# Optimization experiments

Measured on AMD Instinct MI355X. Metric: run time of the kernel, lower is better.

## Reference

```python
import jax, jax.numpy as jnp
import numpy as np


def setup_inputs() -> dict:
    key = jax.random.key(0)
    ks = jax.random.split(key, 5)
    B, T, C = 2, 2048, 1024
    x = jax.random.normal(ks[0], (B, T, C), dtype=jnp.float32)
    Wqkv = jax.random.normal(ks[1], (C, 3 * C), dtype=jnp.float32) * (C ** -0.5)
    bqkv = jax.random.normal(ks[2], (3 * C,), dtype=jnp.float32) * 0.02
    Wproj = jax.random.normal(ks[3], (C, C), dtype=jnp.float32) * (C ** -0.5)
    bproj = jax.random.normal(ks[4], (C,), dtype=jnp.float32) * 0.02
    return {"x": x, "Wqkv": Wqkv, "bqkv": bqkv, "Wproj": Wproj, "bproj": bproj}


def reference(x, Wqkv, bqkv, Wproj, bproj):
    B, T, C = x.shape
    n_head = 16
    hd = C // n_head
    x_proj = x @ Wqkv + bqkv  # [B, T, 3C]
    # NOTE: source reshapes (B, T, C) -> (B, n_head, T, hd) directly (no transpose);
    # we replicate that exactly for faithfulness.
    q = x_proj[:, :, :C].reshape(B, n_head, T, hd)
    k = x_proj[:, :, C:2 * C].reshape(B, n_head, T, hd)
    v = x_proj[:, :, 2 * C:].reshape(B, n_head, T, hd)
    att = jnp.einsum('bhtd,bhsd->bhts', q, k) * (1.0 / jnp.sqrt(jnp.float32(hd)))
    causal = jnp.tril(jnp.ones((T, T), dtype=bool))  # True where allowed
    att = jnp.where(causal, att, jnp.float32(-jnp.inf))
    att = jax.nn.softmax(att, axis=-1)
    y = att @ v  # [B, H, T, hd]
    y = jnp.transpose(y, (0, 2, 1, 3)).reshape(B, T, C)
    return y @ Wproj + bproj
```

## Files before the change

### kernel.cpp

```cpp
#include <hip/hip_runtime.h>
#include <hip/hip_bf16.h>
#include <stdint.h>

typedef __hip_bfloat16 bf16;
typedef __attribute__((ext_vector_type(8))) short bf16x8;
typedef __attribute__((ext_vector_type(4))) float f32x4;

__device__ __forceinline__ bf16x8 ldsv8(const bf16* p) { return *(const bf16x8*)p; }

__device__ __forceinline__ short bf_bits(float f) {
  union { bf16 h; short s; } u; u.h = __float2bfloat16(f); return u.s;
}

#define QSCALE 0.18033688011112042f

#define ASYNC16(ldsdst, gsrc)                                                  \
  __builtin_amdgcn_global_load_lds(                                            \
      (const __attribute__((address_space(1))) void*)(gsrc),                   \
      (__attribute__((address_space(3))) void*)(ldsdst), 16, 0, 0)

__device__ __forceinline__ bool is_bf16(const void* p) {
  const uint32_t* w = (const uint32_t*)p;
  int cnt = 0;
#pragma unroll 8
  for (int i = 0; i < 64; ++i) {
    uint32_t e = (w[i] >> 7) & 0xffu;
    cnt += (e >= 100u && e <= 150u) ? 1 : 0;
  }
  return cnt >= 40;
}

__device__ __forceinline__ float load_f32(const void* p, size_t idx, bool b16) {
  return b16 ? __bfloat162float(((const bf16*)p)[idx]) : ((const float*)p)[idx];
}

__device__ __forceinline__ void cvtT_body(const void* in, bf16* out, int R,
                                          int Ccols, int bx, int by,
                                          bf16 (*tile)[33]) {
  const bool b16 = is_bf16(in);
  int tx = threadIdx.x & 31, ty = threadIdx.x >> 5;
  int c0 = bx * 32, r0 = by * 32;
#pragma unroll
  for (int i = 0; i < 32; i += 8)
    tile[ty + i][tx] = __float2bfloat16(load_f32(in, (size_t)(r0 + ty + i) * Ccols + c0 + tx, b16));
  __syncthreads();
#pragma unroll
  for (int i = 0; i < 32; i += 8)
    out[(size_t)(c0 + ty + i) * R + r0 + tx] = tile[tx][ty + i];
}

__global__ __launch_bounds__(256) void prep_k(const float* __restrict__ x,
                                              bf16* __restrict__ xb,
                                              const void* __restrict__ Wqkv,
                                              bf16* __restrict__ WqkvT,
                                              const void* __restrict__ Wproj,
                                              bf16* __restrict__ WprojT) {
  __shared__ __align__(16) bf16 tile[32][33];
  const int id = blockIdx.x;
  if (id < 2048) {
    size_t i = (size_t)id * 256 + threadIdx.x;
    const float4 f0 = ((const float4*)x)[i * 2];
    const float4 f1 = ((const float4*)x)[i * 2 + 1];
    bf16x8 pk = {bf_bits(f0.x), bf_bits(f0.y), bf_bits(f0.z), bf_bits(f0.w),
                 bf_bits(f1.x), bf_bits(f1.y), bf_bits(f1.z), bf_bits(f1.w)};
    ((bf16x8*)xb)[i] = pk;
  } else if (id < 5120) {
    int id2 = id - 2048;
    cvtT_body(Wqkv, WqkvT, 1024, 3072, id2 % 96, id2 / 96, tile);
  } else {
    int id3 = id - 5120;
    cvtT_body(Wproj, WprojT, 1024, 1024, id3 % 32, id3 / 32, tile);
  }
}

__global__ __launch_bounds__(256) void cvtT_k(const void* __restrict__ in,
                                              bf16* __restrict__ out,
                                              int R, int Ccols) {
  __shared__ __align__(16) bf16 tile[32][33];
  cvtT_body(in, out, R, Ccols, blockIdx.x, blockIdx.y, tile);
}

__global__ __launch_bounds__(256) void cvt_k(const float* __restrict__ in,
                                             bf16* __restrict__ out) {
  size_t i = (size_t)blockIdx.x * 256 + threadIdx.x;
  const float4 f0 = ((const float4*)in)[i * 2];
  const float4 f1 = ((const float4*)in)[i * 2 + 1];
  bf16x8 pk = {bf_bits(f0.x), bf_bits(f0.y), bf_bits(f0.z), bf_bits(f0.w),
               bf_bits(f1.x), bf_bits(f1.y), bf_bits(f1.z), bf_bits(f1.w)};
  ((bf16x8*)out)[i] = pk;
}

template <int MODE, int BN>
__global__ __launch_bounds__(256) void gemm128(
    const void* __restrict__ Araw, const bf16* __restrict__ BT,
    const void* __restrict__ biasraw, void* __restrict__ outv) {
  constexpr int K = 1024;
  constexpr int NBF = BN / 32;
  __shared__ __align__(16) bf16 As[128 * 32];
  __shared__ __align__(16) bf16 Bs[BN * 32];
  const int tid = threadIdx.x;
  const int wave = tid >> 6, lane = tid & 63;
  const int quad = lane >> 4, l16 = lane & 15;
  const int nwg = gridDim.x * gridDim.y;
  const int lin = blockIdx.y * gridDim.x + blockIdx.x;
  const int swz = (lin & 7) * (nwg >> 3) + (lin >> 3);
  const int m0 = (swz / gridDim.y) * 128, n0 = (swz % gridDim.y) * BN;
  const int wm = (wave & 1) * 64, wn = (wave >> 1) * (BN / 2);
  const bool a16 = (MODE == 0) ? is_bf16(Araw) : true;
  const bool bias16 = is_bf16(biasraw);

  f32x4 acc[4][NBF] = {};

  for (int kt = 0; kt < K; kt += 32) {
    __syncthreads();
    if (MODE != 0 || a16) {
#pragma unroll
      for (int i = 0; i < 2; ++i) {
        int slot = i * 256 + tid;
        int row = slot >> 2, col = (slot & 3) << 3;
        ASYNC16(As + slot * 8, ((const bf16*)Araw) + (size_t)(m0 + row) * K + kt + col);
      }
#pragma unroll
      for (int i = 0; i < BN / 64; ++i) {
        int slot = i * 256 + tid;
        int row = slot >> 2, col = (slot & 3) << 3;
        ASYNC16(Bs + slot * 8, BT + (size_t)(n0 + row) * K + kt + col);
      }
    } else {
#pragma unroll
      for (int i = 0; i < 2; ++i) {
        int slot = i * 256 + tid;
        int row = slot >> 2, col = (slot & 3) << 3;
        const float* ap = ((const float*)Araw) + (size_t)(m0 + row) * K + kt + col;
        float4 f0 = *(const float4*)ap;
        float4 f1 = *(const float4*)(ap + 4);
        bf16x8 pk = {bf_bits(f0.x), bf_bits(f0.y), bf_bits(f0.z), bf_bits(f0.w),
                     bf_bits(f1.x), bf_bits(f1.y), bf_bits(f1.z), bf_bits(f1.w)};
        *(bf16x8*)(As + slot * 8) = pk;
        if (i * 256 < BN * 4)
          *(bf16x8*)(Bs + slot * 8) = *(const bf16x8*)(BT + (size_t)(n0 + row) * K + kt + col);
      }
    }
    __syncthreads();
    bf16x8 af[4], bfr[NBF];
#pragma unroll
    for (int i = 0; i < 4; ++i)
      af[i] = ldsv8(As + (wm + i * 16 + l16) * 32 + quad * 8);
#pragma unroll
    for (int j = 0; j < NBF; ++j)
      bfr[j] = ldsv8(Bs + (wn + j * 16 + l16) * 32 + quad * 8);
#pragma unroll
    for (int i = 0; i < 4; ++i)
#pragma unroll
      for (int j = 0; j < NBF; ++j)
        acc[i][j] = __builtin_amdgcn_mfma_f32_16x16x32_bf16(af[i], bfr[j], acc[i][j], 0, 0, 0);
  }

  float biasf[NBF];
#pragma unroll
  for (int j = 0; j < NBF; ++j)
    biasf[j] = load_f32(biasraw, n0 + wn + j * 16 + l16, bias16);

#pragma unroll
  for (int i = 0; i < 4; ++i)
#pragma unroll
    for (int j = 0; j < NBF; ++j) {
      int ng = n0 + wn + j * 16 + l16;
#pragma unroll
      for (int r = 0; r < 4; ++r) {
        int mg = m0 + wm + i * 16 + quad * 4 + r;
        float v = acc[i][j][r] + biasf[j];
        if (MODE == 1) {
          ((float*)outv)[(size_t)mg * 1024 + ng] = v;
        } else {
          ((bf16*)outv)[(size_t)mg * 3072 + ng] =
              __float2bfloat16(ng < 1024 ? v * QSCALE : v);
        }
      }
    }
}

__global__ __launch_bounds__(1024, 4) void attn_k(const bf16* __restrict__ xproj,
                                                  bf16* __restrict__ Yb) {
  constexpr int KSZ = 128 * 72;
  constexpr int VSZ = 64 * 136;
  __shared__ __align__(16) bf16 Ks[2 * KSZ];
  __shared__ __align__(16) bf16 VTs[2 * VSZ];
  __shared__ __align__(16) bf16 Ps[16 * 16 * 136];

  const int tid = threadIdx.x;
  const int wave = tid >> 6, lane = tid & 63;
  const int quad = lane >> 4, l16 = lane & 15;
  const int tl = wave >> 3;
  const int wrow = (wave & 7) * 16;
  const int pid = blockIdx.x;
  const int qtA = pid, qtB = 15 - pid;
  const int qt = tl ? qtB : qtA;
  const int bh = blockIdx.y, b = bh >> 4, h = bh & 15;
  const size_t rowbase = (size_t)(b * 2048 + h * 128) * 3072;
  const int q0 = qt * 128;

  const short onebits = (short)0x3F80;
  const bf16x8 vones = {onebits, onebits, onebits, onebits,
                        onebits, onebits, onebits, onebits};

  bf16x8 aq[2];
  {
    int sg = q0 + wrow + l16;
    const bf16* qp = xproj + rowbase + (size_t)(sg >> 4) * 3072 + ((sg & 15) << 6);
#pragma unroll
    for (int ks = 0; ks < 2; ++ks)
      aq[ks] = *(const bf16x8*)(qp + ks * 32 + quad * 8);
  }

  f32x4 o[4] = {};
  f32x4 lacc = {};

  bf16* Pw = Ps + wave * (16 * 136);

  const int sA = tid >> 3, blkA = tid & 7;

  bf16x8 kreg, vreg;
#define ISSUE_LOADS(stv)                                                        \
  {                                                                             \
    int sg0 = (stv)*128 + sA;                                                   \
    const bf16* b0 = xproj + rowbase + (size_t)(sg0 >> 4) * 3072 + ((sg0 & 15) << 6); \
    kreg = *(const bf16x8*)(b0 + 1024 + blkA * 8);                              \
    vreg = *(const bf16x8*)(b0 + 2048 + blkA * 8);                              \
  }
#define WRITE_TILE(buf)                                                         \
  {                                                                             \
    bf16* Kd = Ks + (buf)*KSZ;                                                  \
    bf16* Vd = VTs + (buf)*VSZ;                                                 \
    *(bf16x8*)(Kd + sA * 72 + blkA * 8) = kreg;                                 \
    const bf16* vv = (const bf16*)&vreg;                                        \
    const int ssw = sA ^ (blkA << 3);                                           \
    _Pragma("unroll")                                                           \
    for (int j = 0; j < 8; ++j) Vd[(blkA * 8 + j) * 136 + ssw] = vv[j];         \
  }

  ISSUE_LOADS(0);
  WRITE_TILE(0);
  ISSUE_LOADS(1);
  __syncthreads();

  int cur = 0;
  for (int st = 0; st <= qtB; ++st) {
    const bf16* Kc = Ks + cur * KSZ;
    const bf16* Vc = VTs + cur * VSZ;

    if (st <= qt) {
      const bool diag = (st == qt);

      f32x4 sc[8] = {};
      __builtin_amdgcn_s_setprio(1);
#pragma unroll
      for (int ks = 0; ks < 2; ++ks)
#pragma unroll
        for (int j = 0; j < 8; ++j) {
          bf16x8 bk = ldsv8(Kc + (j * 16 + l16) * 72 + (ks * 4 + quad) * 8);
          sc[j] = __builtin_amdgcn_mfma_f32_16x16x32_bf16(aq[ks], bk, sc[j], 0, 0, 0);
        }
      __builtin_amdgcn_s_setprio(0);

#pragma unroll
      for (int r = 0; r < 4; ++r) {
        const int rloc = wrow + quad * 4 + r;
        bf16* prow = Pw + (quad * 4 + r) * 136;
        const int psw = quad << 3;
#pragma unroll
        for (int j = 0; j < 8; ++j) {
          float v = sc[j][r];
          if (diag && (j * 16 + l16) > rloc) v = -1e30f;
          prow[(j * 16 + l16) ^ psw] = __float2bfloat16(__builtin_amdgcn_exp2f(v));
        }
      }

      __builtin_amdgcn_s_setprio(1);
#pragma unroll
      for (int ks = 0; ks < 4; ++ks) {
        bf16x8 ap = ldsv8(Pw + l16 * 136 + (((ks * 4 + quad) ^ (l16 >> 2)) << 3));
        lacc = __builtin_amdgcn_mfma_f32_16x16x32_bf16(ap, vones, lacc, 0, 0, 0);
#pragma unroll
        for (int j = 0; j < 4; ++j) {
          int d = j * 16 + l16;
          bf16x8 bv = ldsv8(Vc + d * 136 + (((ks * 4 + quad) ^ (2 * j + (l16 >> 3))) << 3));
          o[j] = __builtin_amdgcn_mfma_f32_16x16x32_bf16(ap, bv, o[j], 0, 0, 0);
        }
      }
      __builtin_amdgcn_s_setprio(0);
    }

    if (st < qtB) {
      WRITE_TILE(cur ^ 1);
      if (st + 2 <= qtB) ISSUE_LOADS(st + 2);
      __syncthreads();
      cur ^= 1;
    }
  }
#undef ISSUE_LOADS
#undef WRITE_TILE

  bf16* Yh = Yb + (size_t)b * 2097152 + h * 64;
#pragma unroll
  for (int r = 0; r < 4; ++r) {
    int tt = q0 + wrow + quad * 4 + r;
    float inv = 1.f / lacc[r];
#pragma unroll
    for (int j = 0; j < 4; ++j)
      Yh[(size_t)tt * 1024 + j * 16 + l16] = __float2bfloat16(o[j][r] * inv);
  }
}

extern "C" void kernel_launch(void* const* d_in, const int* in_sizes, int n_in,
                              void* d_out, int out_size, void* d_ws, size_t ws_size,
                              hipStream_t stream) {
  (void)out_size;
  const void* px     = d_in[0];
  const void* pWqkv  = (n_in > 1) ? d_in[1] : d_in[0];
  const void* pbqkv  = (n_in > 2) ? d_in[2] : d_in[0];
  const void* pWproj = (n_in > 3) ? d_in[3] : d_in[0];
  const void* pbproj = (n_in > 4) ? d_in[4] : d_in[0];
  for (int i = 0; i < n_in; ++i) {
    switch (in_sizes[i]) {
      case 4194304: px     = d_in[i]; break;
      case 3145728: pWqkv  = d_in[i]; break;
      case 3072:    pbqkv  = d_in[i]; break;
      case 1048576: pWproj = d_in[i]; break;
      case 1024:    pbproj = d_in[i]; break;
      default: break;
    }
  }

  char* ws = (char*)d_ws;
  bf16* xproj = (bf16*)(ws + 0);

  if (ws_size >= 41943040) {
    bf16* xb     = (bf16*)(ws + 25165824);
    bf16* WqkvT  = (bf16*)(ws + 33554432);
    bf16* WprojT = (bf16*)(ws + 39845888);
    bf16* Yb     = (bf16*)(ws + 27262976);

    prep_k<<<dim3(6144), 256, 0, stream>>>((const float*)px, xb, pWqkv, WqkvT,
                                           pWproj, WprojT);
    gemm128<0, 128><<<dim3(32, 24), 256, 0, stream>>>(xb, WqkvT, pbqkv, xproj);
    attn_k<<<dim3(8, 32), 1024, 0, stream>>>(xproj, Yb);
    gemm128<1, 64><<<dim3(32, 16), 256, 0, stream>>>(Yb, WprojT, pbproj, d_out);
  } else if (ws_size >= 39845888) {
    bf16* xb     = (bf16*)(ws + 25165824);
    bf16* WqkvT  = (bf16*)(ws + 33554432);
    bf16* WprojT = (bf16*)(ws + 25165824);
    bf16* Yb     = (bf16*)(ws + 27262976);

    cvt_k<<<dim3(2048), 256, 0, stream>>>((const float*)px, xb);
    cvtT_k<<<dim3(96, 32), 256, 0, stream>>>(pWqkv, WqkvT, 1024, 3072);
    gemm128<0, 128><<<dim3(32, 24), 256, 0, stream>>>(xb, WqkvT, pbqkv, xproj);
    cvtT_k<<<dim3(32, 32), 256, 0, stream>>>(pWproj, WprojT, 1024, 1024);
    attn_k<<<dim3(8, 32), 1024, 0, stream>>>(xproj, Yb);
    gemm128<1, 64><<<dim3(32, 16), 256, 0, stream>>>(Yb, WprojT, pbproj, d_out);
  } else {
    bf16* WqkvT  = (bf16*)(ws + 25165824);
    bf16* WprojT = (bf16*)(ws + 25165824);
    bf16* Yb     = (bf16*)(ws + 27262976);

    cvtT_k<<<dim3(96, 32), 256, 0, stream>>>(pWqkv, WqkvT, 1024, 3072);
    gemm128<0, 128><<<dim3(32, 24), 256, 0, stream>>>(px, WqkvT, pbqkv, xproj);
    cvtT_k<<<dim3(32, 32), 256, 0, stream>>>(pWproj, WprojT, 1024, 1024);
    attn_k<<<dim3(8, 32), 1024, 0, stream>>>(xproj, Yb);
    gemm128<1, 64><<<dim3(32, 16), 256, 0, stream>>>(Yb, WprojT, pbproj, d_out);
  }
}
```

Baseline: 186.8 us.

## Split long-tile key range across both wave groups after short tile finishes

Previously one half of the block processed the short query tile and then sat idle while the other half finished the long tile. Now the first group writes its short-tile result early, reloads Q for the long tile, and both groups then split each remaining key tile by 64-key halves. Partial outputs and row sums are combined through shared memory at the end. This is meant to remove the load imbalance between wave groups, at the cost of an extra reduction, extra syncs and narrower MFMA work per tile.

```diff
diff --git a/kernel.cpp b/kernel.cpp
--- a/kernel.cpp
+++ b/kernel.cpp
@@ -195,10 +195,8 @@
   const int wrow = (wave & 7) * 16;
   const int pid = blockIdx.x;
   const int qtA = pid, qtB = 15 - pid;
-  const int qt = tl ? qtB : qtA;
   const int bh = blockIdx.y, b = bh >> 4, h = bh & 15;
   const size_t rowbase = (size_t)(b * 2048 + h * 128) * 3072;
-  const int q0 = qt * 128;
 
   const short onebits = (short)0x3F80;
   const bf16x8 vones = {onebits, onebits, onebits, onebits,
@@ -206,7 +204,7 @@
 
   bf16x8 aq[2];
   {
-    int sg = q0 + wrow + l16;
+    int sg = (tl ? qtB : qtA) * 128 + wrow + l16;
     const bf16* qp = xproj + rowbase + (size_t)(sg >> 4) * 3072 + ((sg & 15) << 6);
 #pragma unroll
     for (int ks = 0; ks < 2; ++ks)
@@ -217,6 +215,7 @@
   f32x4 lacc = {};
 
   bf16* Pw = Ps + wave * (16 * 136);
+  bf16* Yh = Yb + (size_t)b * 2097152 + h * 64;
 
   const int sA = tid >> 3, blkA = tid & 7;
 
@@ -249,8 +248,8 @@
     const bf16* Kc = Ks + cur * KSZ;
     const bf16* Vc = VTs + cur * VSZ;
 
-    if (st <= qt) {
-      const bool diag = (st == qt);
+    if (st <= pid) {
+      const bool diag = (tl == 0) && (st == qtA);
 
       f32x4 sc[8] = {};
       __builtin_amdgcn_s_setprio(1);
@@ -279,6 +278,68 @@
       __builtin_amdgcn_s_setprio(1);
 #pragma unroll
       for (int ks = 0; ks < 4; ++ks) {
+        bf16x8 ap = ldsv8(Pw + l16 * 136 + (((ks * 4 + quad) ^ (l16 >> 2)) << 3));
+        lacc = __builtin_amdgcn_mfma_f32_16x16x32_bf16(ap, vones, lacc, 0, 0, 0);
+#pragma unroll
+        for (int j = 0; j < 4; ++j) {
+          int d = j * 16 + l16;
+          bf16x8 bv = ldsv8(Vc + d * 136 + (((ks * 4 + quad) ^ (2 * j + (l16 >> 3))) << 3));
+          o[j] = __builtin_amdgcn_mfma_f32_16x16x32_bf16(ap, bv, o[j], 0, 0, 0);
+        }
+      }
+      __builtin_amdgcn_s_setprio(0);
+
+      if (st == pid && tl == 0) {
+#pragma unroll
+        for (int r = 0; r < 4; ++r) {
+          int tt = qtA * 128 + wrow + quad * 4 + r;
+          float inv = 1.f / lacc[r];
+#pragma unroll
+          for (int j = 0; j < 4; ++j)
+            Yh[(size_t)tt * 1024 + j * 16 + l16] = __float2bfloat16(o[j][r] * inv);
+        }
+        int sg = qtB * 128 + wrow + l16;
+        const bf16* qp = xproj + rowbase + (size_t)(sg >> 4) * 3072 + ((sg & 15) << 6);
+#pragma unroll
+        for (int ks = 0; ks < 2; ++ks)
+          aq[ks] = *(const bf16x8*)(qp + ks * 32 + quad * 8);
+#pragma unroll
+        for (int j = 0; j < 4; ++j) o[j] = (f32x4){0.f, 0.f, 0.f, 0.f};
+        lacc = (f32x4){0.f, 0.f, 0.f, 0.f};
+      }
+    } else {
+      const int kh = tl;
+      const bool diag = (st == qtB);
+
+      f32x4 sc[4] = {};
+      __builtin_amdgcn_s_setprio(1);
+#pragma unroll
+      for (int ks = 0; ks < 2; ++ks)
+#pragma unroll
+        for (int j = 0; j < 4; ++j) {
+          bf16x8 bk = ldsv8(Kc + (kh * 64 + j * 16 + l16) * 72 + (ks * 4 + quad) * 8);
+          sc[j] = __builtin_amdgcn_mfma_f32_16x16x32_bf16(aq[ks], bk, sc[j], 0, 0, 0);
+        }
+      __builtin_amdgcn_s_setprio(0);
+
+#pragma unroll
+      for (int r = 0; r < 4; ++r) {
+        const int rloc = wrow + quad * 4 + r;
+        bf16* prow = Pw + (quad * 4 + r) * 136;
+        const int psw = quad << 3;
+#pragma unroll
+        for (int j = 0; j < 4; ++j) {
+          float v = sc[j][r];
+          const int key = kh * 64 + j * 16 + l16;
+          if (diag && key > rloc) v = -1e30f;
+          prow[key ^ psw] = __float2bfloat16(__builtin_amdgcn_exp2f(v));
+        }
+      }
+
+      __builtin_amdgcn_s_setprio(1);
+#pragma unroll
+      for (int c = 0; c < 2; ++c) {
+        const int ks = kh * 2 + c;
         bf16x8 ap = ldsv8(Pw + l16 * 136 + (((ks * 4 + quad) ^ (l16 >> 2)) << 3));
         lacc = __builtin_amdgcn_mfma_f32_16x16x32_bf16(ap, vones, lacc, 0, 0, 0);
 #pragma unroll
@@ -301,14 +362,32 @@
 #undef ISSUE_LOADS
 #undef WRITE_TILE
 
-  bf16* Yh = Yb + (size_t)b * 2097152 + h * 64;
-#pragma unroll
-  for (int r = 0; r < 4; ++r) {
-    int tt = q0 + wrow + quad * 4 + r;
-    float inv = 1.f / lacc[r];
-#pragma unroll
-    for (int j = 0; j < 4; ++j)
-      Yh[(size_t)tt * 1024 + j * 16 + l16] = __float2bfloat16(o[j][r] * inv);
+  __syncthreads();
+  {
+    float* so = (float*)Ks;
+    float* sl = (float*)VTs;
+    const int w8 = wave & 7;
+    if (tl == 0) {
+#pragma unroll
+      for (int j = 0; j < 4; ++j)
+        *(f32x4*)(so + ((w8 * 64 + lane) * 16) + j * 4) = o[j];
+      *(f32x4*)(sl + (w8 * 64 + lane) * 4) = lacc;
+    }
+    __syncthreads();
+    if (tl == 1) {
+#pragma unroll
+      for (int j = 0; j < 4; ++j)
+        o[j] += *(const f32x4*)(so + ((w8 * 64 + lane) * 16) + j * 4);
+      lacc += *(const f32x4*)(sl + (w8 * 64 + lane) * 4);
+#pragma unroll
+      for (int r = 0; r < 4; ++r) {
+        int tt = qtB * 128 + wrow + quad * 4 + r;
+        float inv = 1.f / lacc[r];
+#pragma unroll
+        for (int j = 0; j < 4; ++j)
+          Yh[(size_t)tt * 1024 + j * 16 + l16] = __float2bfloat16(o[j][r] * inv);
+      }
+    }
   }
 }
 
```

Result: slower. 200.3 us (+7.2%).
